# Kernel optimization log

Measured on AMD Instinct MI355X. Metric: run time of the kernel, lower is better.

The kernel has to match this reference:

```python
import jax, jax.numpy as jnp
import numpy as np

N = 50000      # nodes
E = 800000     # edges (before self loops)
F_IN = 128     # dataset.num_features
HID = 32       # hidden_channels (per GAT head)
HEADS = 4
C = 40         # dataset.num_classes
NEG_SLOPE = 0.2


def setup_inputs() -> dict:
    key = jax.random.key(0)
    ks = jax.random.split(key, 18)
    g = lambda k, shape, fan: jax.random.normal(k, shape, dtype=jnp.float32) / np.sqrt(fan)
    inp = {
        "x": jax.random.normal(ks[0], (N, F_IN), dtype=jnp.float32),
        "edge_index": jax.random.randint(ks[1], (2, E), 0, N, dtype=jnp.int64),
        # GAT layer 1: F_IN -> HEADS*HID
        "gat_W1": g(ks[2], (F_IN, HEADS * HID), F_IN),
        "gat_att_src1": g(ks[3], (HEADS, HID), HID),
        "gat_att_dst1": g(ks[4], (HEADS, HID), HID),
        "gat_b1": jnp.zeros((HEADS * HID,), jnp.float32),
        # GAT layer 2: HEADS*HID -> C, heads=1
        "gat_W2": g(ks[5], (HEADS * HID, C), HEADS * HID),
        "gat_att_src2": g(ks[6], (1, C), C),
        "gat_att_dst2": g(ks[7], (1, C), C),
        "gat_b2": jnp.zeros((C,), jnp.float32),
        # GCN layers
        "gcn_W1": g(ks[8], (F_IN, HID), F_IN),
        "gcn_b1": jnp.zeros((HID,), jnp.float32),
        "gcn_W2": g(ks[9], (HID, C), HID),
        "gcn_b2": jnp.zeros((C,), jnp.float32),
        # final linear: 2C -> C
        "lin_W": g(ks[10], (2 * C, C), 2 * C),
        "lin_b": jnp.zeros((C,), jnp.float32),
        "weight_c": jnp.float32(0.5),
        "weight_t": jnp.float32(0.5),
    }
    return inp


def _add_self_loops(src, dst, n):
    loop = jnp.arange(n, dtype=src.dtype)
    return jnp.concatenate([src, loop]), jnp.concatenate([dst, loop])


def _gat_conv(x, src, dst, n, W, att_src, att_dst, b, heads, out_dim):
    # h: [n, heads, out_dim]
    h = (x @ W).reshape(n, heads, out_dim)
    a_s = jnp.einsum('nhd,hd->nh', h, att_src)   # source-side attention logit
    a_d = jnp.einsum('nhd,hd->nh', h, att_dst)   # target-side attention logit
    e = jax.nn.leaky_relu(a_s[src] + a_d[dst], NEG_SLOPE)  # [E', heads]
    # softmax over incoming edges of each target node (self loops guarantee >=1 edge)
    m = jax.ops.segment_max(e, dst, num_segments=n)
    ex = jnp.exp(e - m[dst])
    s = jax.ops.segment_sum(ex, dst, num_segments=n)
    alpha = ex / s[dst]                          # [E', heads]
    out = jax.ops.segment_sum(h[src] * alpha[..., None], dst, num_segments=n)
    return out.reshape(n, heads * out_dim) + b


def _gcn_conv(x, src, dst, n, W, b):
    h = x @ W
    deg = jax.ops.segment_sum(jnp.ones(src.shape, h.dtype), dst, num_segments=n)
    norm = jax.lax.rsqrt(deg)                    # deg >= 1 (self loops)
    coef = (norm[src] * norm[dst])[:, None]
    return jax.ops.segment_sum(h[src] * coef, dst, num_segments=n) + b


def reference(x, edge_index, gat_W1, gat_att_src1, gat_att_dst1, gat_b1,
              gat_W2, gat_att_src2, gat_att_dst2, gat_b2,
              gcn_W1, gcn_b1, gcn_W2, gcn_b2, lin_W, lin_b,
              weight_c, weight_t):
    n = x.shape[0]
    src, dst = _add_self_loops(edge_index[0], edge_index[1], n)
    # GAT branch (dropout is identity at inference)
    x_gat = _gat_conv(x, src, dst, n, gat_W1, gat_att_src1, gat_att_dst1,
                      gat_b1, HEADS, HID)
    x_gat = jax.nn.elu(x_gat)
    x_gat = _gat_conv(x_gat, src, dst, n, gat_W2, gat_att_src2, gat_att_dst2,
                      gat_b2, 1, C)
    # GCN branch
    x_gcn = jax.nn.relu(_gcn_conv(x, src, dst, n, gcn_W1, gcn_b1))
    x_gcn = _gcn_conv(x_gcn, src, dst, n, gcn_W2, gcn_b2)
    # weighted feature concat + linear head
    cat = jnp.concatenate([x_gcn * weight_c, x_gat * weight_t], axis=1)  # [n, 2C]
    return cat @ lin_W + lin_b
```

## Files before the change

kernel.cpp:

```cpp
#include <hip/hip_runtime.h>
#include <math.h>

#define F_IN   128
#define HIDC   32
#define NHEAD  4
#define CDIM   40
#define NEG_SLOPE 0.2f
#define BCAP   4096
#define OVCAP  16384
#define SCHUNK 4096

typedef __attribute__((ext_vector_type(8))) short bf16x8;
typedef __attribute__((ext_vector_type(4))) float f32x4;

__device__ __forceinline__ float leakyf(float x) { return x > 0.f ? x : NEG_SLOPE * x; }

__device__ __forceinline__ float wred_sum(float v) {
#pragma unroll
    for (int o = 32; o > 0; o >>= 1) v += __shfl_xor(v, o, 64);
    return v;
}
__device__ __forceinline__ float sel4(float4 v, int h) {
    return (h == 0) ? v.x : (h == 1) ? v.y : (h == 2) ? v.z : v.w;
}
__device__ __forceinline__ unsigned pack2_bf16(float a, float b) {
    unsigned ua = __float_as_uint(a);
    unsigned ub = __float_as_uint(b);
    ua = (ua + 0x7FFFu + ((ua >> 16) & 1u)) >> 16;
    ub = (ub + 0x7FFFu + ((ub >> 16) & 1u)) >> 16;
    return ua | (ub << 16);
}
__device__ __forceinline__ float2 unpack2_bf16(unsigned p) {
    return make_float2(__uint_as_float(p << 16), __uint_as_float(p & 0xFFFF0000u));
}
__device__ __forceinline__ float bf2f(unsigned short u) {
    return __uint_as_float(((unsigned)u) << 16);
}

__global__ void wb_prep_kernel(const float* __restrict__ Wg, const float* __restrict__ Wc,
                               uint4* __restrict__ wbf)
{
    int b = blockIdx.x;
    int lane = threadIdx.x;
    int nt = b >> 2, ks = b & 3;
    int c = nt * 16 + (lane & 15);
    int k0 = ks * 32 + (lane >> 4) * 8;
    unsigned u[4];
#pragma unroll
    for (int jj = 0; jj < 4; ++jj) {
        int k = k0 + 2 * jj;
        float a0 = (c < 128) ? Wg[(size_t)k * 128 + c] : Wc[(size_t)k * 32 + (c - 128)];
        float a1 = (c < 128) ? Wg[(size_t)(k + 1) * 128 + c] : Wc[(size_t)(k + 1) * 32 + (c - 128)];
        u[jj] = pack2_bf16(a0, a1);
    }
    wbf[(size_t)b * 64 + lane] = make_uint4(u[0], u[1], u[2], u[3]);
}

__global__ __launch_bounds__(256) void gemm1_mfma_kernel(
    const float* __restrict__ X, const uint4* __restrict__ wbf,
    const float* __restrict__ aw_s, const float* __restrict__ aw_d,
    unsigned* __restrict__ h1b, unsigned* __restrict__ g1b,
    float* __restrict__ as1, float* __restrict__ ad1, int n)
{
    __shared__ float Ct[64][164];
    __shared__ float sw[128], dw[128];
    const int tid = threadIdx.x;
    const int w = tid >> 6, lane = tid & 63;
    const int m = lane & 15, q = lane >> 4;
    const int node0 = blockIdx.x * 64;
    if (tid < 128) { sw[tid] = aw_s[tid]; dw[tid] = aw_d[tid]; }

    f32x4 acc[10];
#pragma unroll
    for (int t = 0; t < 10; ++t) acc[t] = (f32x4){0.f, 0.f, 0.f, 0.f};

    const int row = node0 + w * 16 + m;
    const bool rv = row < n;
#pragma unroll
    for (int ks = 0; ks < 4; ++ks) {
        uint4 pa = make_uint4(0u, 0u, 0u, 0u);
        if (rv) {
            const float* xr = X + (size_t)row * 128 + ks * 32 + q * 8;
            float4 a0 = *(const float4*)xr;
            float4 a1 = *(const float4*)(xr + 4);
            pa = make_uint4(pack2_bf16(a0.x, a0.y), pack2_bf16(a0.z, a0.w),
                            pack2_bf16(a1.x, a1.y), pack2_bf16(a1.z, a1.w));
        }
        bf16x8 af = *(bf16x8*)&pa;
#pragma unroll
        for (int nt = 0; nt < 10; ++nt) {
            uint4 pb = wbf[(size_t)(nt * 4 + ks) * 64 + lane];
            bf16x8 bfv = *(bf16x8*)&pb;
            acc[nt] = __builtin_amdgcn_mfma_f32_16x16x32_bf16(af, bfv, acc[nt], 0, 0, 0);
        }
    }
#pragma unroll
    for (int nt = 0; nt < 10; ++nt)
#pragma unroll
        for (int r = 0; r < 4; ++r)
            Ct[w * 16 + q * 4 + r][nt * 16 + m] = acc[nt][r];
    __syncthreads();

    for (int i = tid; i < 64 * 64; i += 256) {
        int nd = i >> 6, u = i & 63;
        int gn = node0 + nd;
        if (gn < n)
            h1b[(size_t)gn * 64 + u] = pack2_bf16(Ct[nd][2 * u], Ct[nd][2 * u + 1]);
    }
    for (int i = tid; i < 64 * 16; i += 256) {
        int nd = i >> 4, u = i & 15;
        int gn = node0 + nd;
        if (gn < n)
            g1b[(size_t)gn * 16 + u] = pack2_bf16(Ct[nd][128 + 2 * u], Ct[nd][128 + 2 * u + 1]);
    }
    {
        int nd = tid >> 2, h = tid & 3;
        int gn = node0 + nd;
        if (gn < n) {
            float s = 0.f, d = 0.f;
#pragma unroll
            for (int k = 0; k < HIDC; ++k) {
                float v = Ct[nd][h * HIDC + k];
                s = fmaf(v, sw[h * HIDC + k], s);
                d = fmaf(v, dw[h * HIDC + k], d);
            }
            as1[(size_t)gn * 4 + h] = s;
            ad1[(size_t)gn * 4 + h] = d;
        }
    }
}

template<int K, int OUTC, int BN, int BK, int OSTRIDE = OUTC>
__global__ __launch_bounds__((OUTC / 4) * (BN / 4)) void gemm_tile(
    const float* __restrict__ X, const float* __restrict__ W,
    const float* __restrict__ bias, float* __restrict__ Y, int n)
{
    constexpr int CG = OUTC / 4;
    constexpr int NG = BN / 4;
    constexpr int NT = CG * NG;
    __shared__ float Xs[BK][BN + 4];
    __shared__ float Ws[BK][OUTC];
    const int tid = threadIdx.x;
    const int cg = tid % CG, ng = tid / CG;
    const int node0 = blockIdx.x * BN;
    float acc[4][4] = {};

    for (int kb = 0; kb < K; kb += BK) {
        for (int idx = tid; idx < BN * (BK / 4); idx += NT) {
            int nd = idx / (BK / 4);
            int kq = idx % (BK / 4);
            int gnode = node0 + nd;
            float4 v = (gnode < n) ? *(const float4*)&X[(size_t)gnode * K + kb + kq * 4]
                                   : make_float4(0.f, 0.f, 0.f, 0.f);
            Xs[kq * 4 + 0][nd] = v.x;
            Xs[kq * 4 + 1][nd] = v.y;
            Xs[kq * 4 + 2][nd] = v.z;
            Xs[kq * 4 + 3][nd] = v.w;
        }
        for (int idx = tid; idx < BK * CG; idx += NT) {
            int kk = idx / CG;
            int cq = idx % CG;
            *(float4*)&Ws[kk][cq * 4] = *(const float4*)&W[(size_t)(kb + kk) * OUTC + cq * 4];
        }
        __syncthreads();
#pragma unroll
        for (int k = 0; k < BK; ++k) {
            float4 xv = *(const float4*)&Xs[k][ng * 4];
            float4 wv = *(const float4*)&Ws[k][cg * 4];
            float xa[4] = {xv.x, xv.y, xv.z, xv.w};
            float wa[4] = {wv.x, wv.y, wv.z, wv.w};
#pragma unroll
            for (int j = 0; j < 4; ++j)
#pragma unroll
                for (int c = 0; c < 4; ++c)
                    acc[j][c] = fmaf(xa[j], wa[c], acc[j][c]);
        }
        __syncthreads();
    }

    float4 bv = make_float4(0.f, 0.f, 0.f, 0.f);
    if (bias) bv = *(const float4*)&bias[cg * 4];
#pragma unroll
    for (int j = 0; j < 4; ++j) {
        int gnode = node0 + ng * 4 + j;
        if (gnode < n) {
            float4 o = make_float4(acc[j][0] + bv.x, acc[j][1] + bv.y,
                                   acc[j][2] + bv.z, acc[j][3] + bv.w);
            *(float4*)&Y[(size_t)gnode * OSTRIDE + cg * 4] = o;
        }
    }
}

template<int K, int OUTC, int BN, int BK, int OSTRIDE_U, int OFF_U>
__global__ __launch_bounds__((OUTC / 4) * (BN / 4)) void gemm_tile_bb(
    const unsigned* __restrict__ Xb, const float* __restrict__ W,
    unsigned* __restrict__ Yb, int n)
{
    constexpr int CG = OUTC / 4;
    constexpr int NG = BN / 4;
    constexpr int NT = CG * NG;
    __shared__ float Xs[BK][BN + 4];
    __shared__ float Ws[BK][OUTC];
    const int tid = threadIdx.x;
    const int cg = tid % CG, ng = tid / CG;
    const int node0 = blockIdx.x * BN;
    float acc[4][4] = {};

    for (int kb = 0; kb < K; kb += BK) {
        for (int idx = tid; idx < BN * (BK / 8); idx += NT) {
            int nd = idx / (BK / 8);
            int kq = idx % (BK / 8);
            int gnode = node0 + nd;
            uint4 v = (gnode < n) ? *(const uint4*)&Xb[(size_t)gnode * (K / 2) + kb / 2 + kq * 4]
                                  : make_uint4(0u, 0u, 0u, 0u);
            float2 a = unpack2_bf16(v.x), b = unpack2_bf16(v.y);
            float2 c = unpack2_bf16(v.z), d = unpack2_bf16(v.w);
            Xs[kq * 8 + 0][nd] = a.x; Xs[kq * 8 + 1][nd] = a.y;
            Xs[kq * 8 + 2][nd] = b.x; Xs[kq * 8 + 3][nd] = b.y;
            Xs[kq * 8 + 4][nd] = c.x; Xs[kq * 8 + 5][nd] = c.y;
            Xs[kq * 8 + 6][nd] = d.x; Xs[kq * 8 + 7][nd] = d.y;
        }
        for (int idx = tid; idx < BK * CG; idx += NT) {
            int kk = idx / CG;
            int cq = idx % CG;
            *(float4*)&Ws[kk][cq * 4] = *(const float4*)&W[(size_t)(kb + kk) * OUTC + cq * 4];
        }
        __syncthreads();
#pragma unroll
        for (int k = 0; k < BK; ++k) {
            float4 xv = *(const float4*)&Xs[k][ng * 4];
            float4 wv = *(const float4*)&Ws[k][cg * 4];
            float xa[4] = {xv.x, xv.y, xv.z, xv.w};
            float wa[4] = {wv.x, wv.y, wv.z, wv.w};
#pragma unroll
            for (int j = 0; j < 4; ++j)
#pragma unroll
                for (int c = 0; c < 4; ++c)
                    acc[j][c] = fmaf(xa[j], wa[c], acc[j][c]);
        }
        __syncthreads();
    }

#pragma unroll
    for (int j = 0; j < 4; ++j) {
        int gnode = node0 + ng * 4 + j;
        if (gnode < n) {
            uint2 pb = make_uint2(pack2_bf16(acc[j][0], acc[j][1]),
                                  pack2_bf16(acc[j][2], acc[j][3]));
            *(uint2*)&Yb[(size_t)gnode * OSTRIDE_U + OFF_U + cg * 2] = pb;
        }
    }
}

__global__ __launch_bounds__(320) void gemm2_gat_kernel(
    const unsigned* __restrict__ Xb, const float* __restrict__ W,
    const float* __restrict__ aw_s, const float* __restrict__ aw_d,
    unsigned* __restrict__ Yb, float* __restrict__ as2, float* __restrict__ ad2, int n)
{
    constexpr int K = 128, OUTC = 40, BN = 128, BK = 32;
    constexpr int CG = OUTC / 4, NT = 320;
    __shared__ float smem[32 * 132 + 32 * 40];
    float* Xs = smem;
    float* Ws = smem + 32 * 132;
    const int tid = threadIdx.x;
    const int cg = tid % CG, ng = tid / CG;
    const int node0 = blockIdx.x * BN;
// ... 75 lines not shown
    __shared__ unsigned hist[512];
    __shared__ unsigned base[512];
    const int t = threadIdx.x;
    const int lo = blockIdx.x * SCHUNK;
    const int hi = min(lo + SCHUNK, e);
    for (int i = t; i < nbuck; i += 256) hist[i] = 0;
    __syncthreads();
    for (int i = lo + t; i < hi; i += 256)
        atomicAdd(&hist[((unsigned)dst[i]) >> 7], 1u);
    __syncthreads();
    for (int i = t; i < nbuck; i += 256) {
        unsigned c = hist[i];
        base[i] = c ? atomicAdd(&bcnt[i], c) : 0u;
        hist[i] = 0;
    }
    __syncthreads();
    for (int i = lo + t; i < hi; i += 256) {
        unsigned s = (unsigned)src[i], d = (unsigned)dst[i];
        unsigned b = d >> 7;
        unsigned pos = base[b] + atomicAdd(&hist[b], 1u);
        if (pos < BCAP) bpair[(size_t)b * BCAP + pos] = s | ((d & 127u) << 16);
        else {
            unsigned o = atomicAdd(ovf_cnt, 1u);
            if (o < OVCAP) ovf[o] = make_uint2(s, d);
        }
    }
}

__global__ __launch_bounds__(256) void bucket_count_kernel(
    const unsigned* __restrict__ bcnt, const unsigned* __restrict__ bpair,
    const unsigned* __restrict__ ovf_cnt, const uint2* __restrict__ ovf,
    unsigned* __restrict__ counts, int n)
{
    __shared__ unsigned lc[128];
    const int b = blockIdx.x, base = b << 7;
    if (threadIdx.x < 128) lc[threadIdx.x] = 0;
    __syncthreads();
    unsigned bc = bcnt[b];
    int cnt = (int)(bc < BCAP ? bc : BCAP);
    for (int k = threadIdx.x; k < cnt; k += 256)
        atomicAdd(&lc[bpair[(size_t)b * BCAP + k] >> 16], 1u);
    unsigned oc_u = *ovf_cnt;
    int oc = (int)(oc_u < OVCAP ? oc_u : OVCAP);
    for (int k = threadIdx.x; k < oc; k += 256) {
        uint2 pp = ovf[k];
        if ((int)(pp.y >> 7) == b) atomicAdd(&lc[pp.y & 127u], 1u);
    }
    __syncthreads();
    int i = base + threadIdx.x;
    if (threadIdx.x < 128 && i < n) counts[i] = lc[threadIdx.x];
}

__global__ __launch_bounds__(256) void scan_reduce_kernel(const unsigned* __restrict__ counts,
                                                          unsigned* __restrict__ partials, int n)
{
    __shared__ unsigned sm[256];
    int t = threadIdx.x;
    int i = blockIdx.x * 256 + t;
    unsigned v = (i < n) ? counts[i] : 0u;
    sm[t] = v;
    __syncthreads();
#pragma unroll
    for (int off = 128; off > 0; off >>= 1) {
        if (t < off) sm[t] += sm[t + off];
        __syncthreads();
    }
    if (t == 0) partials[blockIdx.x] = sm[0];
}

__global__ __launch_bounds__(256) void scan_partials_kernel(unsigned* __restrict__ partials,
                                                            unsigned* __restrict__ rs, int nb, int n)
{
    __shared__ unsigned sm[256];
    int t = threadIdx.x;
    unsigned v = (t < nb) ? partials[t] : 0u;
    sm[t] = v;
    __syncthreads();
#pragma unroll
    for (int off = 1; off < 256; off <<= 1) {
        unsigned u = (t >= off) ? sm[t - off] : 0u;
        __syncthreads();
        sm[t] += u;
        __syncthreads();
    }
    if (t < nb) partials[t] = sm[t] - v;
    if (t == 255) rs[n] = sm[255];
}

__global__ __launch_bounds__(256) void scan_write_kernel(const unsigned* __restrict__ counts,
                                                         const unsigned* __restrict__ partials,
                                                         unsigned* __restrict__ rs,
                                                         float* __restrict__ nrm, int n)
{
    __shared__ unsigned sm[256];
    int t = threadIdx.x;
    int i = blockIdx.x * 256 + t;
    unsigned c = (i < n) ? counts[i] : 0u;
    sm[t] = c;
    __syncthreads();
#pragma unroll
    for (int off = 1; off < 256; off <<= 1) {
        unsigned u = (t >= off) ? sm[t - off] : 0u;
        __syncthreads();
        sm[t] += u;
        __syncthreads();
    }
    if (i < n) {
        rs[i] = partials[blockIdx.x] + sm[t] - c;
        nrm[i] = rsqrtf((float)(c + 1u));
    }
}

__global__ __launch_bounds__(256) void bucket_place_kernel(
    const unsigned* __restrict__ bcnt, const unsigned* __restrict__ bpair,
    const unsigned* __restrict__ rs, unsigned* __restrict__ csr_src,
    unsigned* __restrict__ cursor, int n)
{
    __shared__ unsigned lc[128];
    __shared__ unsigned rbase[128];
    const int b = blockIdx.x, base = b << 7;
    if (threadIdx.x < 128) {
        lc[threadIdx.x] = 0;
        int i = base + threadIdx.x;
        rbase[threadIdx.x] = (i < n) ? rs[i] : 0u;
    }
    __syncthreads();
    unsigned bc = bcnt[b];
    int cnt = (int)(bc < BCAP ? bc : BCAP);
    for (int k = threadIdx.x; k < cnt; k += 256) {
        unsigned v = bpair[(size_t)b * BCAP + k];
        unsigned ld = v >> 16;
        unsigned r = atomicAdd(&lc[ld], 1u);
        csr_src[rbase[ld] + r] = v & 0xFFFFu;
    }
    __syncthreads();
    int i = base + threadIdx.x;
    if (threadIdx.x < 128 && i < n) cursor[i] = rbase[threadIdx.x] + lc[threadIdx.x];
}

__global__ void overflow_fill_kernel(const unsigned* __restrict__ ovf_cnt,
                                     const uint2* __restrict__ ovf,
                                     unsigned* __restrict__ cursor,
                                     unsigned* __restrict__ csr_src)
{
    unsigned oc_u = *ovf_cnt;
    int oc = (int)(oc_u < OVCAP ? oc_u : OVCAP);
    for (int k = threadIdx.x; k < oc; k += 256) {
        uint2 pp = ovf[k];
        unsigned pos = atomicAdd(&cursor[pp.y], 1u);
        csr_src[pos] = pp.x;
    }
}

#define CAP1 96
__global__ __launch_bounds__(256) void agg1_fused_kernel(
    const unsigned* __restrict__ h1b, const unsigned* __restrict__ g1b,
    const float* __restrict__ as1, const float* __restrict__ ad1,
    const float* __restrict__ nrm,
    const unsigned* __restrict__ rs, const unsigned* __restrict__ csr_src,
    const float* __restrict__ gat_b1, const float* __restrict__ gcn_b1,
    unsigned* __restrict__ xgb, unsigned* __restrict__ gaccb, int n)
{
    __shared__ unsigned sidx[4][CAP1];
    __shared__ float    w4[4][CAP1][4];
    __shared__ float    cfs[4][CAP1];
    const int wid = threadIdx.x >> 6;
    const int lane = threadIdx.x & 63;
    const int i = blockIdx.x * 4 + wid;
    if (i >= n) return;
    const unsigned beg = rs[i];
    const int deg = (int)(rs[i + 1] - beg);
    const float4* as1v = (const float4*)as1;
    float4 av = as1v[i];
    float4 dv = ((const float4*)ad1)[i];
    const float ni = nrm[i];
    float4 ese = make_float4(__expf(leakyf(av.x + dv.x)), __expf(leakyf(av.y + dv.y)),
                             __expf(leakyf(av.z + dv.z)), __expf(leakyf(av.w + dv.w)));
    float s0 = 0.f, s1 = 0.f, s2 = 0.f, s3 = 0.f;
    for (int k = lane; k < deg; k += 64) {
        unsigned s = csr_src[beg + k];
        float4 a = as1v[s];
        float w0 = __expf(leakyf(a.x + dv.x)), w1 = __expf(leakyf(a.y + dv.y));
        float w2 = __expf(leakyf(a.z + dv.z)), w3 = __expf(leakyf(a.w + dv.w));
        if (k < CAP1) {
            sidx[wid][k] = s;
            *(float4*)&w4[wid][k][0] = make_float4(w0, w1, w2, w3);
            cfs[wid][k] = nrm[s] * ni;
        }
        s0 += w0; s1 += w1; s2 += w2; s3 += w3;
    }
    const int dc  = deg < CAP1 ? deg : CAP1;
    const int dc4 = (dc + 3) & ~3;
    if (lane < dc4 - dc) {
        int k = dc + lane;
        sidx[wid][k] = (unsigned)i;
        *(float4*)&w4[wid][k][0] = make_float4(0.f, 0.f, 0.f, 0.f);
        cfs[wid][k] = 0.f;
    }
    if (lane == 0) { s0 += ese.x; s1 += ese.y; s2 += ese.z; s3 += ese.w; }
    s0 = wred_sum(s0); s1 = wred_sum(s1); s2 = wred_sum(s2); s3 = wred_sum(s3);
    __threadfence_block();

    const int e = lane >> 4, c = lane & 15;
    const int h = c >> 2;
    const float ssh = sel4(make_float4(s0, s1, s2, s3), h);
    const int e2 = lane >> 2, c2 = lane & 3;
    const bool gact = lane < 16;
    const uint4* h1v = (const uint4*)h1b;
    const uint4* g1v = (const uint4*)g1b;

    float acc[8], gacc[8];
#pragma unroll
    for (int t = 0; t < 8; ++t) { acc[t] = 0.f; gacc[t] = 0.f; }

    if (e == 0) {
        uint4 hv = h1v[(size_t)i * 16 + c];
        float wself = sel4(ese, h);
        float2 p0 = unpack2_bf16(hv.x), p1 = unpack2_bf16(hv.y);
        float2 p2 = unpack2_bf16(hv.z), p3 = unpack2_bf16(hv.w);
        acc[0] = p0.x * wself; acc[1] = p0.y * wself;
        acc[2] = p1.x * wself; acc[3] = p1.y * wself;
        acc[4] = p2.x * wself; acc[5] = p2.y * wself;
        acc[6] = p3.x * wself; acc[7] = p3.y * wself;
    }
    if (lane < 4) {
        uint4 gv = g1v[(size_t)i * 4 + lane];
        float w2s = ni * ni;
        float2 q0 = unpack2_bf16(gv.x), q1 = unpack2_bf16(gv.y);
        float2 q2 = unpack2_bf16(gv.z), q3 = unpack2_bf16(gv.w);
        gacc[0] = q0.x * w2s; gacc[1] = q0.y * w2s;
        gacc[2] = q1.x * w2s; gacc[3] = q1.y * w2s;
        gacc[4] = q2.x * w2s; gacc[5] = q2.y * w2s;
        gacc[6] = q3.x * w2s; gacc[7] = q3.y * w2s;
    }

    for (int j = 0; j < dc4; j += 4) {
        unsigned s = sidx[wid][j + e];
        float    w = w4[wid][j + e][h];
        uint4 hv = h1v[(size_t)s * 16 + c];
        float2 p0 = unpack2_bf16(hv.x), p1 = unpack2_bf16(hv.y);
        float2 p2 = unpack2_bf16(hv.z), p3 = unpack2_bf16(hv.w);
        acc[0] = fmaf(p0.x, w, acc[0]); acc[1] = fmaf(p0.y, w, acc[1]);
        acc[2] = fmaf(p1.x, w, acc[2]); acc[3] = fmaf(p1.y, w, acc[3]);
        acc[4] = fmaf(p2.x, w, acc[4]); acc[5] = fmaf(p2.y, w, acc[5]);
        acc[6] = fmaf(p3.x, w, acc[6]); acc[7] = fmaf(p3.y, w, acc[7]);
        if (gact) {
            unsigned s2 = sidx[wid][j + e2];
            float    cw = cfs[wid][j + e2];
            uint4 gv = g1v[(size_t)s2 * 4 + c2];
            float2 q0 = unpack2_bf16(gv.x), q1 = unpack2_bf16(gv.y);
            float2 q2 = unpack2_bf16(gv.z), q3 = unpack2_bf16(gv.w);
            gacc[0] = fmaf(q0.x, cw, gacc[0]); gacc[1] = fmaf(q0.y, cw, gacc[1]);
            gacc[2] = fmaf(q1.x, cw, gacc[2]); gacc[3] = fmaf(q1.y, cw, gacc[3]);
            gacc[4] = fmaf(q2.x, cw, gacc[4]); gacc[5] = fmaf(q2.y, cw, gacc[5]);
            gacc[6] = fmaf(q3.x, cw, gacc[6]); gacc[7] = fmaf(q3.y, cw, gacc[7]);
        }
    }
    for (int j = CAP1; j < deg; ++j) {
        unsigned s = csr_src[beg + j];
        if (e == 0) {
            float4 a = as1v[s];
            float w = __expf(leakyf(sel4(a, h) + sel4(dv, h)));
            uint4 hv = h1v[(size_t)s * 16 + c];
            float2 p0 = unpack2_bf16(hv.x), p1 = unpack2_bf16(hv.y);
            float2 p2 = unpack2_bf16(hv.z), p3 = unpack2_bf16(hv.w);
            acc[0] = fmaf(p0.x, w, acc[0]); acc[1] = fmaf(p0.y, w, acc[1]);
            acc[2] = fmaf(p1.x, w, acc[2]); acc[3] = fmaf(p1.y, w, acc[3]);
            acc[4] = fmaf(p2.x, w, acc[4]); acc[5] = fmaf(p2.y, w, acc[5]);
            acc[6] = fmaf(p3.x, w, acc[6]); acc[7] = fmaf(p3.y, w, acc[7]);
        }
        if (lane < 4) {
            float cw = nrm[s] * ni;
            uint4 gv = g1v[(size_t)s * 4 + lane];
            float2 q0 = unpack2_bf16(gv.x), q1 = unpack2_bf16(gv.y);
            float2 q2 = unpack2_bf16(gv.z), q3 = unpack2_bf16(gv.w);
            gacc[0] = fmaf(q0.x, cw, gacc[0]); gacc[1] = fmaf(q0.y, cw, gacc[1]);
            gacc[2] = fmaf(q1.x, cw, gacc[2]); gacc[3] = fmaf(q1.y, cw, gacc[3]);
            gacc[4] = fmaf(q2.x, cw, gacc[4]); gacc[5] = fmaf(q2.y, cw, gacc[5]);
            gacc[6] = fmaf(q3.x, cw, gacc[6]); gacc[7] = fmaf(q3.y, cw, gacc[7]);
        }
    }

#pragma unroll
    for (int t = 0; t < 8; ++t) {
        acc[t]  += __shfl_xor(acc[t], 16, 64);
        acc[t]  += __shfl_xor(acc[t], 32, 64);
        gacc[t] += __shfl_xor(gacc[t], 4, 64);
        gacc[t] += __shfl_xor(gacc[t], 8, 64);
    }
    if (e == 0) {
        float inv = 1.f / ssh;
        float4 b0 = *(const float4*)&gat_b1[c * 8];
        float4 b1 = *(const float4*)&gat_b1[c * 8 + 4];
        float o[8] = {acc[0] * inv + b0.x, acc[1] * inv + b0.y,
                      acc[2] * inv + b0.z, acc[3] * inv + b0.w,
                      acc[4] * inv + b1.x, acc[5] * inv + b1.y,
                      acc[6] * inv + b1.z, acc[7] * inv + b1.w};
#pragma unroll
        for (int t = 0; t < 8; ++t) o[t] = o[t] > 0.f ? o[t] : __expf(o[t]) - 1.f;
        uint4 pv = make_uint4(pack2_bf16(o[0], o[1]), pack2_bf16(o[2], o[3]),
                              pack2_bf16(o[4], o[5]), pack2_bf16(o[6], o[7]));
        ((uint4*)xgb)[(size_t)i * 16 + c] = pv;
    }
    if (lane < 4) {
        float4 b0 = *(const float4*)&gcn_b1[lane * 8];
        float4 b1 = *(const float4*)&gcn_b1[lane * 8 + 4];
        float g[8] = {fmaxf(gacc[0] + b0.x, 0.f), fmaxf(gacc[1] + b0.y, 0.f),
                      fmaxf(gacc[2] + b0.z, 0.f), fmaxf(gacc[3] + b0.w, 0.f),
                      fmaxf(gacc[4] + b1.x, 0.f), fmaxf(gacc[5] + b1.y, 0.f),
                      fmaxf(gacc[6] + b1.z, 0.f), fmaxf(gacc[7] + b1.w, 0.f)};
        uint4 pv = make_uint4(pack2_bf16(g[0], g[1]), pack2_bf16(g[2], g[3]),
                              pack2_bf16(g[4], g[5]), pack2_bf16(g[6], g[7]));
        ((uint4*)gaccb)[(size_t)i * 4 + lane] = pv;
    }
}

#define CAP2 128
__global__ __launch_bounds__(256) void agg2_fused_kernel(
    const unsigned* __restrict__ hg_b, const float* __restrict__ as2,
    const float* __restrict__ ad2, const float* __restrict__ nrm,
    const unsigned* __restrict__ rs, const unsigned* __restrict__ csr_src,
    const float* __restrict__ gat_b2, const float* __restrict__ gcn_b2,
    const float* __restrict__ wc_p, const float* __restrict__ wt_p,
    float* __restrict__ cat, int n)
{
    __shared__ unsigned sidx[4][CAP2];
    __shared__ float    wgt[4][CAP2];
    __shared__ float    cfn[4][CAP2];
    const int wid = threadIdx.x >> 6;
    const int lane = threadIdx.x & 63;
    const int i = blockIdx.x * 4 + wid;
    if (i >= n) return;
    const unsigned beg = rs[i];
    const int deg = (int)(rs[i + 1] - beg);
    const float adv = ad2[i];
    const float eself = __expf(leakyf(as2[i] + adv));
    const float ni = nrm[i];
    float ssum = (lane == 0) ? eself : 0.f;
    for (int k = lane; k < deg; k += 64) {
        unsigned s = csr_src[beg + k];
        float w = __expf(leakyf(as2[s] + adv));
        if (k < CAP2) { sidx[wid][k] = s; wgt[wid][k] = w; cfn[wid][k] = nrm[s] * ni; }
        ssum += w;
    }
    const int dc  = deg < CAP2 ? deg : CAP2;
    const int dc4 = (dc + 3) & ~3;
    if (lane < dc4 - dc) {
        int k = dc + lane;
        sidx[wid][k] = (unsigned)i; wgt[wid][k] = 0.f; cfn[wid][k] = 0.f;
    }
    ssum = wred_sum(ssum);
    __threadfence_block();

    const int e = lane & 3, c = lane >> 2;
    const bool act = c < 10;
    const bool isgat = c < 5;
    const float* wptr = isgat ? &wgt[wid][0] : &cfn[wid][0];
    const uint4* hgv = (const uint4*)hg_b;

    float acc[8];
#pragma unroll
    for (int t = 0; t < 8; ++t) acc[t] = 0.f;
    if (act && e == 0) {
        uint4 hv = hgv[(size_t)i * 10 + c];
        float sw = isgat ? eself : ni * ni;
        float2 p0 = unpack2_bf16(hv.x), p1 = unpack2_bf16(hv.y);
        float2 p2 = unpack2_bf16(hv.z), p3 = unpack2_bf16(hv.w);
        acc[0] = p0.x * sw; acc[1] = p0.y * sw;
        acc[2] = p1.x * sw; acc[3] = p1.y * sw;
        acc[4] = p2.x * sw; acc[5] = p2.y * sw;
        acc[6] = p3.x * sw; acc[7] = p3.y * sw;
    }
    if (act) {
        for (int j = 0; j < dc4; j += 4) {
            unsigned s = sidx[wid][j + e];
            float    w = wptr[j + e];
            uint4 hv = hgv[(size_t)s * 10 + c];
            float2 p0 = unpack2_bf16(hv.x), p1 = unpack2_bf16(hv.y);
            float2 p2 = unpack2_bf16(hv.z), p3 = unpack2_bf16(hv.w);
            acc[0] = fmaf(p0.x, w, acc[0]); acc[1] = fmaf(p0.y, w, acc[1]);
            acc[2] = fmaf(p1.x, w, acc[2]); acc[3] = fmaf(p1.y, w, acc[3]);
            acc[4] = fmaf(p2.x, w, acc[4]); acc[5] = fmaf(p2.y, w, acc[5]);
            acc[6] = fmaf(p3.x, w, acc[6]); acc[7] = fmaf(p3.y, w, acc[7]);
        }
        for (int j = CAP2; j < deg; ++j) {
            if (e == 0) {
                unsigned s = csr_src[beg + j];
                float w = isgat ? __expf(leakyf(as2[s] + adv)) : nrm[s] * ni;
                uint4 hv = hgv[(size_t)s * 10 + c];
                float2 p0 = unpack2_bf16(hv.x), p1 = unpack2_bf16(hv.y);
                float2 p2 = unpack2_bf16(hv.z), p3 = unpack2_bf16(hv.w);
                acc[0] = fmaf(p0.x, w, acc[0]); acc[1] = fmaf(p0.y, w, acc[1]);
                acc[2] = fmaf(p1.x, w, acc[2]); acc[3] = fmaf(p1.y, w, acc[3]);
                acc[4] = fmaf(p2.x, w, acc[4]); acc[5] = fmaf(p2.y, w, acc[5]);
                acc[6] = fmaf(p3.x, w, acc[6]); acc[7] = fmaf(p3.y, w, acc[7]);
            }
        }
    }
#pragma unroll
    for (int t = 0; t < 8; ++t) {
        acc[t] += __shfl_xor(acc[t], 1, 64);
        acc[t] += __shfl_xor(acc[t], 2, 64);
    }
    if (act && e == 0) {
        if (isgat) {
            float inv = 1.f / ssum, wt = *wt_p;
            float4 b0 = *(const float4*)&gat_b2[c * 8];
            float4 b1 = *(const float4*)&gat_b2[c * 8 + 4];
            float4 o0 = make_float4((acc[0] * inv + b0.x) * wt, (acc[1] * inv + b0.y) * wt,
                                    (acc[2] * inv + b0.z) * wt, (acc[3] * inv + b0.w) * wt);
            float4 o1 = make_float4((acc[4] * inv + b1.x) * wt, (acc[5] * inv + b1.y) * wt,
                                    (acc[6] * inv + b1.z) * wt, (acc[7] * inv + b1.w) * wt);
            *(float4*)&cat[(size_t)i * 80 + 40 + c * 8]     = o0;
            *(float4*)&cat[(size_t)i * 80 + 40 + c * 8 + 4] = o1;
        } else {
            float wc = *wc_p;
            int g = c - 5;
            float4 b0 = *(const float4*)&gcn_b2[g * 8];
            float4 b1 = *(const float4*)&gcn_b2[g * 8 + 4];
            float4 o0 = make_float4((acc[0] + b0.x) * wc, (acc[1] + b0.y) * wc,
                                    (acc[2] + b0.z) * wc, (acc[3] + b0.w) * wc);
            float4 o1 = make_float4((acc[4] + b1.x) * wc, (acc[5] + b1.y) * wc,
                                    (acc[6] + b1.z) * wc, (acc[7] + b1.w) * wc);
            *(float4*)&cat[(size_t)i * 80 + g * 8]     = o0;
            *(float4*)&cat[(size_t)i * 80 + g * 8 + 4] = o1;
        }
    }
}

extern "C" void kernel_launch(void* const* d_in, const int* in_sizes, int n_in,
                              void* d_out, int out_size, void* d_ws, size_t ws_size,
                              hipStream_t stream)
{
    const float* x        = (const float*)d_in[0];
    const int*   eidx     = (const int*)d_in[1];
    const float* gat_W1   = (const float*)d_in[2];
    const float* att_s1   = (const float*)d_in[3];
    const float* att_d1   = (const float*)d_in[4];
    const float* gat_b1   = (const float*)d_in[5];
    const float* gat_W2   = (const float*)d_in[6];
    const float* att_s2   = (const float*)d_in[7];
    const float* att_d2   = (const float*)d_in[8];
    const float* gat_b2   = (const float*)d_in[9];
    const float* gcn_W1   = (const float*)d_in[10];
    const float* gcn_b1   = (const float*)d_in[11];
    const float* gcn_W2   = (const float*)d_in[12];
    const float* gcn_b2   = (const float*)d_in[13];
    const float* lin_W    = (const float*)d_in[14];
    const float* lin_b    = (const float*)d_in[15];
    const float* wc_p     = (const float*)d_in[16];
    const float* wt_p     = (const float*)d_in[17];

    const int n = in_sizes[0] / F_IN;
    const int e = in_sizes[1] / 2;
    const int* src = eidx;
    const int* dst = eidx + e;
    const int NBUCK = (n + 127) >> 7;

    char* p = (char*)d_ws;
    auto alloc = [&](size_t bytes) -> void* {
        void* r = (void*)p;
        p += (bytes + 255) & ~(size_t)255;
        return r;
    };
    unsigned* counts  = (unsigned*)alloc((size_t)n * 4);
    unsigned* rs      = (unsigned*)alloc((size_t)(n + 1) * 4);
    unsigned* cursor  = (unsigned*)alloc((size_t)n * 4);
    unsigned* partials= (unsigned*)alloc(256 * 4);
    unsigned* bcnt    = (unsigned*)alloc((size_t)(NBUCK + 1) * 4);
    unsigned* csr_src = (unsigned*)alloc((size_t)e * 4);
    uint4*    wbf     = (uint4*)alloc(40 * 64 * 16);
    float* nrm     = (float*)alloc((size_t)n * 4);
    float* as1     = (float*)alloc((size_t)n * 4 * 4);
    float* ad1     = (float*)alloc((size_t)n * 4 * 4);
    float* as2     = (float*)alloc((size_t)n * 4);
    float* ad2     = (float*)alloc((size_t)n * 4);
    float* cat     = (float*)alloc((size_t)n * 80 * 4);
    unsigned* hg_b = (unsigned*)alloc((size_t)n * 40 * 4);
    float* xg      = (float*)alloc((size_t)n * F_IN * 4);
    unsigned* g1b  = (unsigned*)alloc((size_t)n * 16 * 4);
    unsigned* gaccb= (unsigned*)alloc((size_t)n * 16 * 4);
    unsigned* bpair = (unsigned*)cat;
    uint2*    ovf   = (uint2*)(bpair + (size_t)NBUCK * BCAP);
    unsigned* h1b   = (unsigned*)cat;
    unsigned* xgb   = (unsigned*)xg;
    unsigned* ovf_cnt = bcnt + NBUCK;

    const int NB = (n + 255) / 256;
    const int WB = (n + 3) / 4;
    const int SB = (e + SCHUNK - 1) / SCHUNK;

    hipMemsetAsync(bcnt, 0, (size_t)(NBUCK + 1) * 4, stream);
    bucket_scatter_kernel<<<SB, 256, 0, stream>>>(src, dst, bcnt, bpair, ovf_cnt, ovf, e, NBUCK);
    bucket_count_kernel<<<NBUCK, 256, 0, stream>>>(bcnt, bpair, ovf_cnt, ovf, counts, n);
    scan_reduce_kernel<<<NB, 256, 0, stream>>>(counts, partials, n);
    scan_partials_kernel<<<1, 256, 0, stream>>>(partials, rs, NB, n);
    scan_write_kernel<<<NB, 256, 0, stream>>>(counts, partials, rs, nrm, n);
    bucket_place_kernel<<<NBUCK, 256, 0, stream>>>(bcnt, bpair, rs, csr_src, cursor, n);
    overflow_fill_kernel<<<1, 256, 0, stream>>>(ovf_cnt, ovf, cursor, csr_src);

    wb_prep_kernel<<<40, 64, 0, stream>>>(gat_W1, gcn_W1, wbf);
    gemm1_mfma_kernel<<<(n + 63) / 64, 256, 0, stream>>>(x, wbf, att_s1, att_d1,
                                                         h1b, g1b, as1, ad1, n);

    agg1_fused_kernel<<<WB, 256, 0, stream>>>(h1b, g1b, as1, ad1, nrm, rs, csr_src,
                                              gat_b1, gcn_b1, xgb, gaccb, n);

    gemm_tile_bb<32, 40, 128, 32, 40, 20><<<(n + 127) / 128, 320, 0, stream>>>(gaccb, gcn_W2, hg_b, n);
    gemm2_gat_kernel<<<(n + 127) / 128, 320, 0, stream>>>(xgb, gat_W2, att_s2, att_d2,
                                                          hg_b, as2, ad2, n);

    agg2_fused_kernel<<<WB, 256, 0, stream>>>(hg_b, as2, ad2, nrm, rs, csr_src,
                                              gat_b2, gcn_b2, wc_p, wt_p, cat, n);

    gemm_tile<80, 40, 128, 40><<<(n + 127) / 128, 320, 0, stream>>>(cat, lin_W, lin_b, (float*)d_out, n);
}
```

Baseline: 309.8 us.

## Single-pass register-prefetched aggregation with interleaved GAT/GCN feature rows

Both aggregation kernels drop the two-pass scheme that staged source indices and softmax weights in shared memory. Each wave now loads up to 64 neighbor indices into registers, broadcasts them with shuffles, and computes weights inline while software-prefetching the next neighbor's features. The softmax denominator is accumulated in the same pass. Layer-1 GAT and GCN features are packed into one 80-word row per node so both come from the same row, and high-degree tails are processed four edges at a time instead of serially. The cost is extra register pressure and recomputing expf per lane group.

```diff
diff --git a/kernel.cpp b/kernel.cpp
--- a/kernel.cpp
+++ b/kernel.cpp
@@ -15,11 +15,6 @@
 
 __device__ __forceinline__ float leakyf(float x) { return x > 0.f ? x : NEG_SLOPE * x; }
 
-__device__ __forceinline__ float wred_sum(float v) {
-#pragma unroll
-    for (int o = 32; o > 0; o >>= 1) v += __shfl_xor(v, o, 64);
-    return v;
-}
 __device__ __forceinline__ float sel4(float4 v, int h) {
     return (h == 0) ? v.x : (h == 1) ? v.y : (h == 2) ? v.z : v.w;
 }
@@ -33,9 +28,6 @@
 __device__ __forceinline__ float2 unpack2_bf16(unsigned p) {
     return make_float2(__uint_as_float(p << 16), __uint_as_float(p & 0xFFFF0000u));
 }
-__device__ __forceinline__ float bf2f(unsigned short u) {
-    return __uint_as_float(((unsigned)u) << 16);
-}
 
 __global__ void wb_prep_kernel(const float* __restrict__ Wg, const float* __restrict__ Wc,
                                uint4* __restrict__ wbf)
@@ -59,7 +51,7 @@
 __global__ __launch_bounds__(256) void gemm1_mfma_kernel(
     const float* __restrict__ X, const uint4* __restrict__ wbf,
     const float* __restrict__ aw_s, const float* __restrict__ aw_d,
-    unsigned* __restrict__ h1b, unsigned* __restrict__ g1b,
+    unsigned* __restrict__ hb,
     float* __restrict__ as1, float* __restrict__ ad1, int n)
 {
     __shared__ float Ct[64][164];
@@ -105,13 +97,13 @@
         int nd = i >> 6, u = i & 63;
         int gn = node0 + nd;
         if (gn < n)
-            h1b[(size_t)gn * 64 + u] = pack2_bf16(Ct[nd][2 * u], Ct[nd][2 * u + 1]);
+            hb[(size_t)gn * 80 + u] = pack2_bf16(Ct[nd][2 * u], Ct[nd][2 * u + 1]);
     }
     for (int i = tid; i < 64 * 16; i += 256) {
         int nd = i >> 4, u = i & 15;
         int gn = node0 + nd;
         if (gn < n)
-            g1b[(size_t)gn * 16 + u] = pack2_bf16(Ct[nd][128 + 2 * u], Ct[nd][128 + 2 * u + 1]);
+            hb[(size_t)gn * 80 + 64 + u] = pack2_bf16(Ct[nd][128 + 2 * u], Ct[nd][128 + 2 * u + 1]);
     }
     {
         int nd = tid >> 2, h = tid & 3;
@@ -493,18 +485,14 @@
     }
 }
 
-#define CAP1 96
 __global__ __launch_bounds__(256) void agg1_fused_kernel(
-    const unsigned* __restrict__ h1b, const unsigned* __restrict__ g1b,
+    const unsigned* __restrict__ hb,
     const float* __restrict__ as1, const float* __restrict__ ad1,
     const float* __restrict__ nrm,
     const unsigned* __restrict__ rs, const unsigned* __restrict__ csr_src,
     const float* __restrict__ gat_b1, const float* __restrict__ gcn_b1,
     unsigned* __restrict__ xgb, unsigned* __restrict__ gaccb, int n)
 {
-    __shared__ unsigned sidx[4][CAP1];
-    __shared__ float    w4[4][CAP1][4];
-    __shared__ float    cfs[4][CAP1];
     const int wid = threadIdx.x >> 6;
     const int lane = threadIdx.x & 63;
     const int i = blockIdx.x * 4 + wid;
@@ -512,83 +500,112 @@
     const unsigned beg = rs[i];
     const int deg = (int)(rs[i + 1] - beg);
     const float4* as1v = (const float4*)as1;
-    float4 av = as1v[i];
-    float4 dv = ((const float4*)ad1)[i];
-    const float ni = nrm[i];
-    float4 ese = make_float4(__expf(leakyf(av.x + dv.x)), __expf(leakyf(av.y + dv.y)),
-                             __expf(leakyf(av.z + dv.z)), __expf(leakyf(av.w + dv.w)));
-    float s0 = 0.f, s1 = 0.f, s2 = 0.f, s3 = 0.f;
-    for (int k = lane; k < deg; k += 64) {
-        unsigned s = csr_src[beg + k];
-        float4 a = as1v[s];
-        float w0 = __expf(leakyf(a.x + dv.x)), w1 = __expf(leakyf(a.y + dv.y));
-        float w2 = __expf(leakyf(a.z + dv.z)), w3 = __expf(leakyf(a.w + dv.w));
-        if (k < CAP1) {
-            sidx[wid][k] = s;
-            *(float4*)&w4[wid][k][0] = make_float4(w0, w1, w2, w3);
-            cfs[wid][k] = nrm[s] * ni;
-        }
-        s0 += w0; s1 += w1; s2 += w2; s3 += w3;
-    }
-    const int dc  = deg < CAP1 ? deg : CAP1;
-    const int dc4 = (dc + 3) & ~3;
-    if (lane < dc4 - dc) {
-        int k = dc + lane;
-        sidx[wid][k] = (unsigned)i;
-        *(float4*)&w4[wid][k][0] = make_float4(0.f, 0.f, 0.f, 0.f);
-        cfs[wid][k] = 0.f;
-    }
-    if (lane == 0) { s0 += ese.x; s1 += ese.y; s2 += ese.z; s3 += ese.w; }
-    s0 = wred_sum(s0); s1 = wred_sum(s1); s2 = wred_sum(s2); s3 = wred_sum(s3);
-    __threadfence_block();
+    const uint4*  hv4  = (const uint4*)hb;
 
     const int e = lane >> 4, c = lane & 15;
     const int h = c >> 2;
-    const float ssh = sel4(make_float4(s0, s1, s2, s3), h);
-    const int e2 = lane >> 2, c2 = lane & 3;
-    const bool gact = lane < 16;
-    const uint4* h1v = (const uint4*)h1b;
-    const uint4* g1v = (const uint4*)g1b;
+    const bool gc = c < 4;
+
+    const float4 dv = ((const float4*)ad1)[i];
+    const float dvh = sel4(dv, h);
+    const float ni  = nrm[i];
+
+    unsigned pre = (lane < deg) ? csr_src[beg + lane] : (unsigned)i;
+
+    const float4 av = as1v[i];
+    const float eself = __expf(leakyf(sel4(av, h) + dvh));
 
     float acc[8], gacc[8];
 #pragma unroll
     for (int t = 0; t < 8; ++t) { acc[t] = 0.f; gacc[t] = 0.f; }
+    float sumw = 0.f;
 
     if (e == 0) {
-        uint4 hv = h1v[(size_t)i * 16 + c];
-        float wself = sel4(ese, h);
+        uint4 hv = hv4[(size_t)i * 20 + c];
         float2 p0 = unpack2_bf16(hv.x), p1 = unpack2_bf16(hv.y);
         float2 p2 = unpack2_bf16(hv.z), p3 = unpack2_bf16(hv.w);
-        acc[0] = p0.x * wself; acc[1] = p0.y * wself;
-        acc[2] = p1.x * wself; acc[3] = p1.y * wself;
-        acc[4] = p2.x * wself; acc[5] = p2.y * wself;
-        acc[6] = p3.x * wself; acc[7] = p3.y * wself;
-    }
-    if (lane < 4) {
-        uint4 gv = g1v[(size_t)i * 4 + lane];
-        float w2s = ni * ni;
-        float2 q0 = unpack2_bf16(gv.x), q1 = unpack2_bf16(gv.y);
-        float2 q2 = unpack2_bf16(gv.z), q3 = unpack2_bf16(gv.w);
-        gacc[0] = q0.x * w2s; gacc[1] = q0.y * w2s;
-        gacc[2] = q1.x * w2s; gacc[3] = q1.y * w2s;
-        gacc[4] = q2.x * w2s; gacc[5] = q2.y * w2s;
-        gacc[6] = q3.x * w2s; gacc[7] = q3.y * w2s;
-    }
-
-    for (int j = 0; j < dc4; j += 4) {
-        unsigned s = sidx[wid][j + e];
-        float    w = w4[wid][j + e][h];
-        uint4 hv = h1v[(size_t)s * 16 + c];
+        acc[0] = p0.x * eself; acc[1] = p0.y * eself;
+        acc[2] = p1.x * eself; acc[3] = p1.y * eself;
+        acc[4] = p2.x * eself; acc[5] = p2.y * eself;
+        acc[6] = p3.x * eself; acc[7] = p3.y * eself;
+        if (gc) {
+            uint4 gv = hv4[(size_t)i * 20 + 16 + c];
+            float w2s = ni * ni;
+            float2 q0 = unpack2_bf16(gv.x), q1 = unpack2_bf16(gv.y);
+            float2 q2 = unpack2_bf16(gv.z), q3 = unpack2_bf16(gv.w);
+            gacc[0] = q0.x * w2s; gacc[1] = q0.y * w2s;
+            gacc[2] = q1.x * w2s; gacc[3] = q1.y * w2s;
+            gacc[4] = q2.x * w2s; gacc[5] = q2.y * w2s;
+            gacc[6] = q3.x * w2s; gacc[7] = q3.y * w2s;
+        }
+    }
+
+    const int dfast = deg < 64 ? deg : 64;
+    const int steps = (dfast + 3) >> 2;
+
+    float4 a_cur = make_float4(0.f, 0.f, 0.f, 0.f);
+    uint4  h_cur = make_uint4(0u, 0u, 0u, 0u);
+    uint4  g_cur = make_uint4(0u, 0u, 0u, 0u);
+    float  nr_cur = 0.f;
+    if (steps > 0) {
+        unsigned s = __shfl(pre, e, 64);
+        if (e >= deg) s = (unsigned)i;
+        a_cur = as1v[s];
+        h_cur = hv4[(size_t)s * 20 + c];
+        if (gc) { g_cur = hv4[(size_t)s * 20 + 16 + c]; nr_cur = nrm[s]; }
+    }
+    for (int j = 0; j < steps; ++j) {
+        float4 a_nxt = a_cur;
+        uint4  h_nxt = h_cur, g_nxt = g_cur;
+        float  nr_nxt = nr_cur;
+        if (j + 1 < steps) {
+            int idx = (j + 1) * 4 + e;
+            unsigned s = __shfl(pre, idx, 64);
+            if (idx >= deg) s = (unsigned)i;
+            a_nxt = as1v[s];
+            h_nxt = hv4[(size_t)s * 20 + c];
+            if (gc) { g_nxt = hv4[(size_t)s * 20 + 16 + c]; nr_nxt = nrm[s]; }
+        }
+        const bool val = (j * 4 + e) < deg;
+        float w = __expf(leakyf(sel4(a_cur, h) + dvh));
+        w = val ? w : 0.f;
+        sumw += w;
+        {
+            float2 p0 = unpack2_bf16(h_cur.x), p1 = unpack2_bf16(h_cur.y);
+            float2 p2 = unpack2_bf16(h_cur.z), p3 = unpack2_bf16(h_cur.w);
+            acc[0] = fmaf(p0.x, w, acc[0]); acc[1] = fmaf(p0.y, w, acc[1]);
+            acc[2] = fmaf(p1.x, w, acc[2]); acc[3] = fmaf(p1.y, w, acc[3]);
+            acc[4] = fmaf(p2.x, w, acc[4]); acc[5] = fmaf(p2.y, w, acc[5]);
+            acc[6] = fmaf(p3.x, w, acc[6]); acc[7] = fmaf(p3.y, w, acc[7]);
+        }
+        if (gc) {
+            float cw = val ? nr_cur * ni : 0.f;
+            float2 q0 = unpack2_bf16(g_cur.x), q1 = unpack2_bf16(g_cur.y);
+            float2 q2 = unpack2_bf16(g_cur.z), q3 = unpack2_bf16(g_cur.w);
+            gacc[0] = fmaf(q0.x, cw, gacc[0]); gacc[1] = fmaf(q0.y, cw, gacc[1]);
+            gacc[2] = fmaf(q1.x, cw, gacc[2]); gacc[3] = fmaf(q1.y, cw, gacc[3]);
+            gacc[4] = fmaf(q2.x, cw, gacc[4]); gacc[5] = fmaf(q2.y, cw, gacc[5]);
+            gacc[6] = fmaf(q3.x, cw, gacc[6]); gacc[7] = fmaf(q3.y, cw, gacc[7]);
+        }
+        a_cur = a_nxt; h_cur = h_nxt; g_cur = g_nxt; nr_cur = nr_nxt;
+    }
+    for (int j4 = 64; j4 < deg; j4 += 4) {
+        int idx = j4 + e;
+        bool val = idx < deg;
+        unsigned s = val ? csr_src[beg + idx] : (unsigned)i;
+        float4 a = as1v[s];
+        float w = val ? __expf(leakyf(sel4(a, h) + dvh)) : 0.f;
+        sumw += w;
+        uint4 hv = hv4[(size_t)s * 20 + c];
         float2 p0 = unpack2_bf16(hv.x), p1 = unpack2_bf16(hv.y);
         float2 p2 = unpack2_bf16(hv.z), p3 = unpack2_bf16(hv.w);
         acc[0] = fmaf(p0.x, w, acc[0]); acc[1] = fmaf(p0.y, w, acc[1]);
         acc[2] = fmaf(p1.x, w, acc[2]); acc[3] = fmaf(p1.y, w, acc[3]);
         acc[4] = fmaf(p2.x, w, acc[4]); acc[5] = fmaf(p2.y, w, acc[5]);
         acc[6] = fmaf(p3.x, w, acc[6]); acc[7] = fmaf(p3.y, w, acc[7]);
-        if (gact) {
-            unsigned s2 = sidx[wid][j + e2];
-            float    cw = cfs[wid][j + e2];
-            uint4 gv = g1v[(size_t)s2 * 4 + c2];
+        if (gc) {
+            float cw = val ? nrm[s] * ni : 0.f;
+            uint4 gv = hv4[(size_t)s * 20 + 16 + c];
             float2 q0 = unpack2_bf16(gv.x), q1 = unpack2_bf16(gv.y);
             float2 q2 = unpack2_bf16(gv.z), q3 = unpack2_bf16(gv.w);
             gacc[0] = fmaf(q0.x, cw, gacc[0]); gacc[1] = fmaf(q0.y, cw, gacc[1]);
@@ -597,38 +614,18 @@
             gacc[6] = fmaf(q3.x, cw, gacc[6]); gacc[7] = fmaf(q3.y, cw, gacc[7]);
         }
     }
-    for (int j = CAP1; j < deg; ++j) {
-        unsigned s = csr_src[beg + j];
-        if (e == 0) {
-            float4 a = as1v[s];
-            float w = __expf(leakyf(sel4(a, h) + sel4(dv, h)));
-            uint4 hv = h1v[(size_t)s * 16 + c];
-            float2 p0 = unpack2_bf16(hv.x), p1 = unpack2_bf16(hv.y);
-            float2 p2 = unpack2_bf16(hv.z), p3 = unpack2_bf16(hv.w);
-            acc[0] = fmaf(p0.x, w, acc[0]); acc[1] = fmaf(p0.y, w, acc[1]);
-            acc[2] = fmaf(p1.x, w, acc[2]); acc[3] = fmaf(p1.y, w, acc[3]);
-            acc[4] = fmaf(p2.x, w, acc[4]); acc[5] = fmaf(p2.y, w, acc[5]);
-            acc[6] = fmaf(p3.x, w, acc[6]); acc[7] = fmaf(p3.y, w, acc[7]);
-        }
-        if (lane < 4) {
-            float cw = nrm[s] * ni;
-            uint4 gv = g1v[(size_t)s * 4 + lane];
-            float2 q0 = unpack2_bf16(gv.x), q1 = unpack2_bf16(gv.y);
-            float2 q2 = unpack2_bf16(gv.z), q3 = unpack2_bf16(gv.w);
-            gacc[0] = fmaf(q0.x, cw, gacc[0]); gacc[1] = fmaf(q0.y, cw, gacc[1]);
-            gacc[2] = fmaf(q1.x, cw, gacc[2]); gacc[3] = fmaf(q1.y, cw, gacc[3]);
-            gacc[4] = fmaf(q2.x, cw, gacc[4]); gacc[5] = fmaf(q2.y, cw, gacc[5]);
-            gacc[6] = fmaf(q3.x, cw, gacc[6]); gacc[7] = fmaf(q3.y, cw, gacc[7]);
-        }
-    }
 
 #pragma unroll
     for (int t = 0; t < 8; ++t) {
         acc[t]  += __shfl_xor(acc[t], 16, 64);
         acc[t]  += __shfl_xor(acc[t], 32, 64);
-        gacc[t] += __shfl_xor(gacc[t], 4, 64);
-        gacc[t] += __shfl_xor(gacc[t], 8, 64);
-    }
+        gacc[t] += __shfl_xor(gacc[t], 16, 64);
+        gacc[t] += __shfl_xor(gacc[t], 32, 64);
+    }
+    sumw += __shfl_xor(sumw, 16, 64);
+    sumw += __shfl_xor(sumw, 32, 64);
+    const float ssh = sumw + eself;
+
     if (e == 0) {
         float inv = 1.f / ssh;
         float4 b0 = *(const float4*)&gat_b1[c * 8];
@@ -642,21 +639,20 @@
         uint4 pv = make_uint4(pack2_bf16(o[0], o[1]), pack2_bf16(o[2], o[3]),
                               pack2_bf16(o[4], o[5]), pack2_bf16(o[6], o[7]));
         ((uint4*)xgb)[(size_t)i * 16 + c] = pv;
-    }
-    if (lane < 4) {
-        float4 b0 = *(const float4*)&gcn_b1[lane * 8];
-        float4 b1 = *(const float4*)&gcn_b1[lane * 8 + 4];
-        float g[8] = {fmaxf(gacc[0] + b0.x, 0.f), fmaxf(gacc[1] + b0.y, 0.f),
-                      fmaxf(gacc[2] + b0.z, 0.f), fmaxf(gacc[3] + b0.w, 0.f),
-                      fmaxf(gacc[4] + b1.x, 0.f), fmaxf(gacc[5] + b1.y, 0.f),
-                      fmaxf(gacc[6] + b1.z, 0.f), fmaxf(gacc[7] + b1.w, 0.f)};
-        uint4 pv = make_uint4(pack2_bf16(g[0], g[1]), pack2_bf16(g[2], g[3]),
-                              pack2_bf16(g[4], g[5]), pack2_bf16(g[6], g[7]));
-        ((uint4*)gaccb)[(size_t)i * 4 + lane] = pv;
-    }
-}
-
-#define CAP2 128
+        if (gc) {
+            float4 c0 = *(const float4*)&gcn_b1[c * 8];
+            float4 c1 = *(const float4*)&gcn_b1[c * 8 + 4];
+            float g[8] = {fmaxf(gacc[0] + c0.x, 0.f), fmaxf(gacc[1] + c0.y, 0.f),
+                          fmaxf(gacc[2] + c0.z, 0.f), fmaxf(gacc[3] + c0.w, 0.f),
+                          fmaxf(gacc[4] + c1.x, 0.f), fmaxf(gacc[5] + c1.y, 0.f),
+                          fmaxf(gacc[6] + c1.z, 0.f), fmaxf(gacc[7] + c1.w, 0.f)};
+            uint4 gv = make_uint4(pack2_bf16(g[0], g[1]), pack2_bf16(g[2], g[3]),
+                                  pack2_bf16(g[4], g[5]), pack2_bf16(g[6], g[7]));
+            ((uint4*)gaccb)[(size_t)i * 4 + c] = gv;
+        }
+    }
+}
+
 __global__ __launch_bounds__(256) void agg2_fused_kernel(
     const unsigned* __restrict__ hg_b, const float* __restrict__ as2,
     const float* __restrict__ ad2, const float* __restrict__ nrm,
@@ -665,43 +661,26 @@
     const float* __restrict__ wc_p, const float* __restrict__ wt_p,
     float* __restrict__ cat, int n)
 {
-    __shared__ unsigned sidx[4][CAP2];
-    __shared__ float    wgt[4][CAP2];
-    __shared__ float    cfn[4][CAP2];
     const int wid = threadIdx.x >> 6;
     const int lane = threadIdx.x & 63;
     const int i = blockIdx.x * 4 + wid;
     if (i >= n) return;
     const unsigned beg = rs[i];
     const int deg = (int)(rs[i + 1] - beg);
+    const int e = lane & 3, c = lane >> 2;
+    const bool act = c < 10, isgat = c < 5;
     const float adv = ad2[i];
+    const float ni = nrm[i];
+    const uint4* hgv = (const uint4*)hg_b;
+
+    unsigned pre = (lane < deg) ? csr_src[beg + lane] : (unsigned)i;
     const float eself = __expf(leakyf(as2[i] + adv));
-    const float ni = nrm[i];
-    float ssum = (lane == 0) ? eself : 0.f;
-    for (int k = lane; k < deg; k += 64) {
-        unsigned s = csr_src[beg + k];
-        float w = __expf(leakyf(as2[s] + adv));
-        if (k < CAP2) { sidx[wid][k] = s; wgt[wid][k] = w; cfn[wid][k] = nrm[s] * ni; }
-        ssum += w;
-    }
-    const int dc  = deg < CAP2 ? deg : CAP2;
-    const int dc4 = (dc + 3) & ~3;
-    if (lane < dc4 - dc) {
-        int k = dc + lane;
-        sidx[wid][k] = (unsigned)i; wgt[wid][k] = 0.f; cfn[wid][k] = 0.f;
-    }
-    ssum = wred_sum(ssum);
-    __threadfence_block();
-
-    const int e = lane & 3, c = lane >> 2;
-    const bool act = c < 10;
-    const bool isgat = c < 5;
-    const float* wptr = isgat ? &wgt[wid][0] : &cfn[wid][0];
-    const uint4* hgv = (const uint4*)hg_b;
 
     float acc[8];
 #pragma unroll
     for (int t = 0; t < 8; ++t) acc[t] = 0.f;
+    float sumw = 0.f;
+
     if (act && e == 0) {
         uint4 hv = hgv[(size_t)i * 10 + c];
         float sw = isgat ? eself : ni * ni;
@@ -712,10 +691,58 @@
         acc[4] = p2.x * sw; acc[5] = p2.y * sw;
         acc[6] = p3.x * sw; acc[7] = p3.y * sw;
     }
-    if (act) {
-        for (int j = 0; j < dc4; j += 4) {
-            unsigned s = sidx[wid][j + e];
-            float    w = wptr[j + e];
+
+    const int dfast = deg < 64 ? deg : 64;
+    const int steps = (dfast + 3) >> 2;
+
+    float aw_cur = 0.f;
+    uint4 h_cur = make_uint4(0u, 0u, 0u, 0u);
+    if (steps > 0) {
+        unsigned s = __shfl(pre, e, 64);
+        if (e >= deg) s = (unsigned)i;
+        if (act) { aw_cur = isgat ? as2[s] : nrm[s]; h_cur = hgv[(size_t)s * 10 + c]; }
+    }
+    for (int j = 0; j < steps; ++j) {
+        float aw_nxt = aw_cur;
+        uint4 h_nxt = h_cur;
+        if (j + 1 < steps) {
+            int idx = (j + 1) * 4 + e;
+            unsigned s = __shfl(pre, idx, 64);
+            if (idx >= deg) s = (unsigned)i;
+            if (act) { aw_nxt = isgat ? as2[s] : nrm[s]; h_nxt = hgv[(size_t)s * 10 + c]; }
+        }
+        const bool val = (j * 4 + e) < deg;
+        float w;
+        if (isgat) {
+            w = __expf(leakyf(aw_cur + adv));
+            w = val ? w : 0.f;
+            sumw += w;
+        } else {
+            w = val ? aw_cur * ni : 0.f;
+        }
+        if (act) {
+            float2 p0 = unpack2_bf16(h_cur.x), p1 = unpack2_bf16(h_cur.y);
+            float2 p2 = unpack2_bf16(h_cur.z), p3 = unpack2_bf16(h_cur.w);
+            acc[0] = fmaf(p0.x, w, acc[0]); acc[1] = fmaf(p0.y, w, acc[1]);
+            acc[2] = fmaf(p1.x, w, acc[2]); acc[3] = fmaf(p1.y, w, acc[3]);
+            acc[4] = fmaf(p2.x, w, acc[4]); acc[5] = fmaf(p2.y, w, acc[5]);
+            acc[6] = fmaf(p3.x, w, acc[6]); acc[7] = fmaf(p3.y, w, acc[7]);
+        }
+        aw_cur = aw_nxt; h_cur = h_nxt;
+    }
+    for (int j4 = 64; j4 < deg; j4 += 4) {
+        int idx = j4 + e;
+        bool val = idx < deg;
+        unsigned s = val ? csr_src[beg + idx] : (unsigned)i;
+        if (act) {
+            float aw = isgat ? as2[s] : nrm[s];
+            float w;
+            if (isgat) {
+                w = val ? __expf(leakyf(aw + adv)) : 0.f;
+                sumw += w;
+            } else {
+                w = val ? aw * ni : 0.f;
+            }
             uint4 hv = hgv[(size_t)s * 10 + c];
             float2 p0 = unpack2_bf16(hv.x), p1 = unpack2_bf16(hv.y);
             float2 p2 = unpack2_bf16(hv.z), p3 = unpack2_bf16(hv.w);
@@ -724,25 +751,17 @@
             acc[4] = fmaf(p2.x, w, acc[4]); acc[5] = fmaf(p2.y, w, acc[5]);
             acc[6] = fmaf(p3.x, w, acc[6]); acc[7] = fmaf(p3.y, w, acc[7]);
         }
-        for (int j = CAP2; j < deg; ++j) {
-            if (e == 0) {
-                unsigned s = csr_src[beg + j];
-                float w = isgat ? __expf(leakyf(as2[s] + adv)) : nrm[s] * ni;
-                uint4 hv = hgv[(size_t)s * 10 + c];
-                float2 p0 = unpack2_bf16(hv.x), p1 = unpack2_bf16(hv.y);
-                float2 p2 = unpack2_bf16(hv.z), p3 = unpack2_bf16(hv.w);
-                acc[0] = fmaf(p0.x, w, acc[0]); acc[1] = fmaf(p0.y, w, acc[1]);
-                acc[2] = fmaf(p1.x, w, acc[2]); acc[3] = fmaf(p1.y, w, acc[3]);
-                acc[4] = fmaf(p2.x, w, acc[4]); acc[5] = fmaf(p2.y, w, acc[5]);
-                acc[6] = fmaf(p3.x, w, acc[6]); acc[7] = fmaf(p3.y, w, acc[7]);
-            }
-        }
-    }
+    }
+
 #pragma unroll
     for (int t = 0; t < 8; ++t) {
         acc[t] += __shfl_xor(acc[t], 1, 64);
         acc[t] += __shfl_xor(acc[t], 2, 64);
     }
+    sumw += __shfl_xor(sumw, 1, 64);
+    sumw += __shfl_xor(sumw, 2, 64);
+    const float ssum = sumw + eself;
+
     if (act && e == 0) {
         if (isgat) {
             float inv = 1.f / ssum, wt = *wt_p;
@@ -819,11 +838,10 @@
     float* cat     = (float*)alloc((size_t)n * 80 * 4);
     unsigned* hg_b = (unsigned*)alloc((size_t)n * 40 * 4);
     float* xg      = (float*)alloc((size_t)n * F_IN * 4);
-    unsigned* g1b  = (unsigned*)alloc((size_t)n * 16 * 4);
     unsigned* gaccb= (unsigned*)alloc((size_t)n * 16 * 4);
     unsigned* bpair = (unsigned*)cat;
     uint2*    ovf   = (uint2*)(bpair + (size_t)NBUCK * BCAP);
-    unsigned* h1b   = (unsigned*)cat;
+    unsigned* hb    = (unsigned*)cat;
     unsigned* xgb   = (unsigned*)xg;
     unsigned* ovf_cnt = bcnt + NBUCK;
 
@@ -842,9 +860,9 @@
 
     wb_prep_kernel<<<40, 64, 0, stream>>>(gat_W1, gcn_W1, wbf);
     gemm1_mfma_kernel<<<(n + 63) / 64, 256, 0, stream>>>(x, wbf, att_s1, att_d1,
-                                                         h1b, g1b, as1, ad1, n);
-
-    agg1_fused_kernel<<<WB, 256, 0, stream>>>(h1b, g1b, as1, ad1, nrm, rs, csr_src,
+                                                         hb, as1, ad1, n);
+
+    agg1_fused_kernel<<<WB, 256, 0, stream>>>(hb, as1, ad1, nrm, rs, csr_src,
                                               gat_b1, gcn_b1, xgb, gaccb, n);
 
     gemm_tile_bb<32, 40, 128, 32, 40, 20><<<(n + 127) / 128, 320, 0, stream>>>(gaccb, gcn_W2, hg_b, n);
```

Result: no change. 306.0 us (-1.2%).
